# Kernel optimization log

Measured on AMD Instinct MI355X. Metric: run time of the kernel, lower is better.

The kernel has to match this reference:

```python
import jax, jax.numpy as jnp
import numpy as np

B, N, C, H = 2, 4096, 512, 8
D = C // H          # head dim = 64
EPS = 1e-5          # nn.LayerNorm default eps


def _layernorm(x, gamma, beta):
    m = jnp.mean(x, axis=-1, keepdims=True)
    v = jnp.var(x, axis=-1, keepdims=True)
    return (x - m) * jax.lax.rsqrt(v + EPS) * gamma + beta


def setup_inputs() -> dict:
    key = jax.random.key(0)
    k_x, k_w = jax.random.split(key, 2)
    return {
        "x": jax.random.normal(k_x, (B, N, C), dtype=jnp.float32),
        "w_qkv": jax.random.normal(k_w, (C, 3 * C), dtype=jnp.float32) * 0.02,
        "b_qkv": jnp.zeros((3 * C,), dtype=jnp.float32),
        "g_pre": jnp.ones((C,), dtype=jnp.float32),
        "beta_pre": jnp.zeros((C,), dtype=jnp.float32),
        "g_post": jnp.ones((C,), dtype=jnp.float32),
        "beta_post": jnp.zeros((C,), dtype=jnp.float32),
    }


def reference(x, w_qkv, b_qkv, g_pre, beta_pre, g_post, beta_post):
    b, n, c = x.shape
    xn = _layernorm(x, g_pre, beta_pre)                       # pre_norm (x is reassigned in source)
    qkv = (xn @ w_qkv + b_qkv).reshape(b, n, 3, H, D)
    qkv = jnp.transpose(qkv, (2, 0, 3, 1, 4))                 # [3, B, H, N, D]
    q, k, v = qkv[0], qkv[1], qkv[2]
    scale = D ** (-0.5)
    attn = jnp.einsum('bhnd,bhmd->bhnm', q, k) * scale        # [B, H, N, N]
    soft = jax.nn.softmax(attn, axis=-1)
    val = jnp.einsum('bhnm,bhmd->bhnd', soft, v)              # [B, H, N, D]
    val = jnp.transpose(val, (0, 2, 1, 3)).reshape(b, n, c)   # [B, N, C]
    val = _layernorm(val, g_post, beta_post)                  # post_norm
    return xn + val                                            # residual uses pre-normed x (faithful)
```

## Files before the change

### kernel.cpp

```cpp
#include <hip/hip_runtime.h>

#define BB   2
#define NN   4096
#define CC   512
#define HH   8
#define DD   64
#define MR   8192
#define NC3  1536
#define PS   4194304

typedef __attribute__((ext_vector_type(8))) short short8;
typedef __attribute__((ext_vector_type(4))) float floatx4;

__device__ inline unsigned short f2bf(float f) {
  unsigned int u = __float_as_uint(f);
  u = (u + 0x7fffu + ((u >> 16) & 1u)) >> 16;
  return (unsigned short)u;
}

__device__ inline unsigned int pack_bf2(float a, float b) {
  unsigned int ua = __float_as_uint(a) + 0x8000u;
  unsigned int ub = __float_as_uint(b) + 0x8000u;
  return (ub & 0xffff0000u) | (ua >> 16);
}

__device__ inline floatx4 fzero4() { floatx4 z = {0.f, 0.f, 0.f, 0.f}; return z; }

__device__ inline void async_cp16(const void* g, void* l) {
  __builtin_amdgcn_global_load_lds(
      (const __attribute__((address_space(1))) unsigned int*)g,
      (__attribute__((address_space(3))) unsigned int*)l, 16, 0, 0);
}

__global__ __launch_bounds__(256) void convert_w_kernel(
    const float* __restrict__ w, unsigned short* __restrict__ wt) {
  __shared__ short T[64][68];
  int bn = blockIdx.x;
  int bk = blockIdx.y;
  int tid = threadIdx.x;
  for (int p = 0; p < 4; p++) {
    int k = p * 16 + (tid >> 4);
    int n4 = (tid & 15) * 4;
    float4 v = *(const float4*)&w[(size_t)(bk * 64 + k) * NC3 + bn * 64 + n4];
    T[n4 + 0][k] = (short)f2bf(v.x);
    T[n4 + 1][k] = (short)f2bf(v.y);
    T[n4 + 2][k] = (short)f2bf(v.z);
    T[n4 + 3][k] = (short)f2bf(v.w);
  }
  __syncthreads();
  for (int p = 0; p < 2; p++) {
    int n = p * 32 + (tid >> 3);
    int k8 = (tid & 7) * 8;
    uint4 v = *(uint4*)&T[n][k8];
    *(uint4*)&wt[(size_t)(bn * 64 + n) * 512 + bk * 64 + k8] = v;
  }
}

__global__ __launch_bounds__(256) void pre_ln_kernel(
    const float* __restrict__ x, const float* __restrict__ g,
    const float* __restrict__ be, float* __restrict__ xn,
    unsigned short* __restrict__ xnb) {
  int wv = threadIdx.x >> 6, lane = threadIdx.x & 63;
  int row = blockIdx.x * 4 + wv;
  const float4* xr = (const float4*)(x + (size_t)row * CC);
  float4 v0 = xr[lane];
  float4 v1 = xr[64 + lane];
  float s  = (v0.x + v0.y) + (v0.z + v0.w) + (v1.x + v1.y) + (v1.z + v1.w);
  float sq = (v0.x * v0.x + v0.y * v0.y) + (v0.z * v0.z + v0.w * v0.w) +
             (v1.x * v1.x + v1.y * v1.y) + (v1.z * v1.z + v1.w * v1.w);
  for (int off = 1; off < 64; off <<= 1) {
    s  += __shfl_xor(s,  off, 64);
    sq += __shfl_xor(sq, off, 64);
  }
  float mean = s * (1.0f / CC);
  float var  = sq * (1.0f / CC) - mean * mean;
  float rstd = rsqrtf(var + 1e-5f);
  const float4* gg = (const float4*)g;
  const float4* bb = (const float4*)be;
  float4 g0 = gg[lane], g1 = gg[64 + lane];
  float4 b0 = bb[lane], b1 = bb[64 + lane];
  float4 o0, o1;
  o0.x = (v0.x - mean) * rstd * g0.x + b0.x;
  o0.y = (v0.y - mean) * rstd * g0.y + b0.y;
  o0.z = (v0.z - mean) * rstd * g0.z + b0.z;
  o0.w = (v0.w - mean) * rstd * g0.w + b0.w;
  o1.x = (v1.x - mean) * rstd * g1.x + b1.x;
  o1.y = (v1.y - mean) * rstd * g1.y + b1.y;
  o1.z = (v1.z - mean) * rstd * g1.z + b1.z;
  o1.w = (v1.w - mean) * rstd * g1.w + b1.w;
  size_t base = (size_t)row * CC;
  ((float4*)(xn + base))[lane] = o0;
  ((float4*)(xn + base))[64 + lane] = o1;
  uint2 u0, u1;
  u0.x = pack_bf2(o0.x, o0.y); u0.y = pack_bf2(o0.z, o0.w);
  u1.x = pack_bf2(o1.x, o1.y); u1.y = pack_bf2(o1.z, o1.w);
  *(uint2*)&xnb[base + 4 * lane] = u0;
  *(uint2*)&xnb[base + 256 + 4 * lane] = u1;
}

#define QSCALE 0.180336879f

__global__ __launch_bounds__(256) void qkv_gemm_kernel(
    const unsigned short* __restrict__ xnb, const unsigned short* __restrict__ wt,
    const float* __restrict__ bias, unsigned short* __restrict__ qkvb) {
  __shared__ __align__(16) char smem[65536];
  short (*Asb[2])[64];
  short (*Bsb[2])[64];
  Asb[0] = (short (*)[64])smem;
  Bsb[0] = (short (*)[64])(smem + 16384);
  Asb[1] = (short (*)[64])(smem + 32768);
  Bsb[1] = (short (*)[64])(smem + 49152);
  short (*T)[136] = (short (*)[136])smem;

  int tn = blockIdx.x;
  int tm = blockIdx.y;
  int tid = threadIdx.x;
  int wv = tid >> 6, lane = tid & 63;
  int quad = lane >> 4, l16 = lane & 15;
  int wm = wv >> 1, wn = wv & 1;
  int l7 = l16 & 7;

  int kr = lane >> 3;
  int kg = (lane & 7) ^ kr;

  floatx4 acc[4][4];
  for (int i = 0; i < 4; i++) for (int j = 0; j < 4; j++) acc[i][j] = fzero4();

  for (int i = 0; i < 4; i++) {
    int rb = i * 32 + wv * 8;
    async_cp16(&xnb[(size_t)(tm * 128 + rb + kr) * 512 + kg * 8], &Asb[0][rb][0]);
    async_cp16(&wt [(size_t)(tn * 128 + rb + kr) * 512 + kg * 8], &Bsb[0][rb][0]);
  }

  for (int it = 0; it < 8; it++) {
    __syncthreads();
    short (*As)[64] = Asb[it & 1];
    short (*Bs)[64] = Bsb[it & 1];
    if (it < 7) {
      int kn = (it + 1) * 64;
      short (*An)[64] = Asb[(it + 1) & 1];
      short (*Bn)[64] = Bsb[(it + 1) & 1];
      for (int i = 0; i < 4; i++) {
        int rb = i * 32 + wv * 8;
        async_cp16(&xnb[(size_t)(tm * 128 + rb + kr) * 512 + kn + kg * 8], &An[rb][0]);
        async_cp16(&wt [(size_t)(tn * 128 + rb + kr) * 512 + kn + kg * 8], &Bn[rb][0]);
      }
    }
    for (int kk = 0; kk < 2; kk++) {
      short8 a[4], b[4];
      for (int mt = 0; mt < 4; mt++)
        a[mt] = *(const short8*)&As[wm * 64 + mt * 16 + l16][((kk * 4 + quad) ^ l7) * 8];
      for (int nt = 0; nt < 4; nt++)
        b[nt] = *(const short8*)&Bs[wn * 64 + nt * 16 + l16][((kk * 4 + quad) ^ l7) * 8];
      for (int mt = 0; mt < 4; mt++)
        for (int nt = 0; nt < 4; nt++)
          acc[mt][nt] = __builtin_amdgcn_mfma_f32_16x16x32_bf16(a[mt], b[nt], acc[mt][nt], 0, 0, 0);
    }
  }
  __syncthreads();

  int part = tn >> 2;
  int b = tm >> 5;
  int tloc = (tm & 31) * 128;

  if (part < 2) {
    for (int nt = 0; nt < 4; nt++) {
      int coll = wn * 64 + nt * 16 + l16;
      float bv = bias[tn * 128 + coll];
      for (int mt = 0; mt < 4; mt++) {
        int rowb = wm * 64 + mt * 16 + quad * 4;
        for (int r = 0; r < 4; r++) {
          float v = acc[mt][nt][r] + bv;
          if (part == 0) v *= QSCALE;
          T[rowb + r][coll] = (short)f2bf(v);
        }
      }
    }
    __syncthreads();
    int h0 = (tn & 3) * 2;
    for (int it = 0; it < 8; it++) {
      int row = it * 16 + (tid >> 4);
      int l = tid & 15;
      uint4 vv = *(uint4*)&T[row][l * 8];
      int h = h0 + (l >> 3), d = (l & 7) * 8;
      size_t idx = (size_t)part * PS +
                   ((size_t)((b * 8 + h) * 4096 + tloc + row)) * 64 + d;
      *(uint4*)&qkvb[idx] = vv;
    }
  } else {
    for (int nt = 0; nt < 4; nt++) {
      int coll = wn * 64 + nt * 16 + l16;
      float bv = bias[tn * 128 + coll];
      for (int mt = 0; mt < 4; mt++) {
        int rowb = wm * 64 + mt * 16 + quad * 4;
        uint2 w;
        w.x = pack_bf2(acc[mt][nt][0] + bv, acc[mt][nt][1] + bv);
        w.y = pack_bf2(acc[mt][nt][2] + bv, acc[mt][nt][3] + bv);
        *(uint2*)&T[coll][rowb] = w;
      }
    }
    __syncthreads();
    for (int it = 0; it < 8; it++) {
      int vrow = it * 16 + (tid >> 4);
      int l = tid & 15;
      uint4 vv = *(uint4*)&T[vrow][l * 8];
      int gj = tn * 128 + vrow;
      int h = (gj >> 6) & 7, d = gj & 63;
      size_t idx = 2 * (size_t)PS +
                   ((size_t)((b * 8 + h) * 64 + d)) * 4096 + tloc + l * 8;
      *(uint4*)&qkvb[idx] = vv;
    }
  }
}

#define SMEM_ATT (16384 + 32768 + 18432)

__global__ __launch_bounds__(256, 2) void attn_kernel(
    const unsigned short* __restrict__ qkvb, float* __restrict__ val) {
  __shared__ __align__(16) char smem[SMEM_ATT];
  short (*Ks)[64]   = (short (*)[64])smem;
  short (*Vt0)[128] = (short (*)[128])(smem + 16384);
  short (*Vt1)[128] = (short (*)[128])(smem + 32768);
  short (*Psl)[72]  = (short (*)[72])(smem + 49152);
  float (*slab)[68] = (float (*)[68])smem;

  int bh = blockIdx.y;
  int qb = blockIdx.x * 128;
  int tid = threadIdx.x;
  int wv = tid >> 6, lane = tid & 63, quad = lane >> 4, l16 = lane & 15;
  int l7 = l16 & 7;
  const unsigned short* Qg = qkvb + (size_t)bh * NN * DD;
  const unsigned short* Kg = qkvb + (size_t)PS + (size_t)bh * NN * DD;
  const unsigned short* Vg = qkvb + 2 * (size_t)PS + (size_t)bh * DD * NN;

  int kr = lane >> 3;
  int kg = (lane & 7) ^ kr;
  int vr = lane >> 4;
  int vgr = (lane & 15) ^ ((wv * 4 + vr) & 15);

  for (int i = 0; i < 4; i++) {
    int rowbase = i * 32 + wv * 8;
    async_cp16(&Qg[(size_t)(qb + rowbase + kr) * 64 + kg * 8], &Ks[rowbase][0]);
  }
  __syncthreads();
  short8 qf[2][2];
  for (int g = 0; g < 2; g++)
    for (int kk = 0; kk < 2; kk++)
      qf[g][kk] = *(const short8*)&Ks[wv * 32 + g * 16 + l16][((kk * 4 + quad) ^ l7) * 8];
  __syncthreads();

  for (int i = 0; i < 4; i++) {
    int rb = i * 32 + wv * 8;
    async_cp16(&Kg[(size_t)(rb + kr) * 64 + kg * 8], &Ks[rb][0]);
  }
  for (int i = 0; i < 4; i++) {
    int rb = i * 16 + wv * 4;
    async_cp16(&Vg[(size_t)(rb + vr) * NN + vgr * 8], &Vt0[rb][0]);
  }

  floatx4 o[2][4];
  for (int g = 0; g < 2; g++) for (int dt = 0; dt < 4; dt++) o[g][dt] = fzero4();
  float ls[2] = {0.0f, 0.0f};

  short* psrow0 = &Psl[wv * 32 + l16][0];
  short* psrow1 = &Psl[wv * 32 + 16 + l16][0];

  for (int kt = 0; kt < 32; kt++) {
    __syncthreads();
    short (*Vc)[128] = (kt & 1) ? Vt1 : Vt0;
    short (*Vn)[128] = (kt & 1) ? Vt0 : Vt1;
    if (kt < 31) {
      int kn = (kt + 1) * 128;
      for (int i = 0; i < 4; i++) {
        int rb = i * 16 + wv * 4;
        async_cp16(&Vg[(size_t)(rb + vr) * NN + kn + vgr * 8], &Vn[rb][0]);
      }
    }

    floatx4 s[2][8];
    for (int nt = 0; nt < 8; nt++) {
      short8 kf0 = *(const short8*)&Ks[nt * 16 + l16][((quad) ^ l7) * 8];
      short8 kf1 = *(const short8*)&Ks[nt * 16 + l16][((4 + quad) ^ l7) * 8];
      floatx4 s0 = fzero4(), s1 = fzero4();
      s0 = __builtin_amdgcn_mfma_f32_16x16x32_bf16(kf0, qf[0][0], s0, 0, 0, 0);
      s0 = __builtin_amdgcn_mfma_f32_16x16x32_bf16(kf1, qf[0][1], s0, 0, 0, 0);
      s1 = __builtin_amdgcn_mfma_f32_16x16x32_bf16(kf0, qf[1][0], s1, 0, 0, 0);
      s1 = __builtin_amdgcn_mfma_f32_16x16x32_bf16(kf1, qf[1][1], s1, 0, 0, 0);
      s[0][nt] = s0;
      s[1][nt] = s1;
    }
    __syncthreads();
    if (kt < 31) {
      int kn = (kt + 1) * 128;
      for (int i = 0; i < 4; i++) {
        int rb = i * 32 + wv * 8;
        async_cp16(&Kg[(size_t)(kn + rb + kr) * 64 + kg * 8], &Ks[rb][0]);
      }
    }

    for (int hf = 0; hf < 2; hf++) {
      for (int n4 = 0; n4 < 4; n4++) {
        int nt = hf * 4 + n4;
        float p00 = __builtin_amdgcn_exp2f(s[0][nt][0]);
        float p01 = __builtin_amdgcn_exp2f(s[0][nt][1]);
        float p02 = __builtin_amdgcn_exp2f(s[0][nt][2]);
        float p03 = __builtin_amdgcn_exp2f(s[0][nt][3]);
        float p10 = __builtin_amdgcn_exp2f(s[1][nt][0]);
        float p11 = __builtin_amdgcn_exp2f(s[1][nt][1]);
        float p12 = __builtin_amdgcn_exp2f(s[1][nt][2]);
        float p13 = __builtin_amdgcn_exp2f(s[1][nt][3]);
        ls[0] += (p00 + p01) + (p02 + p03);
        ls[1] += (p10 + p11) + (p12 + p13);
        uint2 w0, w1;
        w0.x = pack_bf2(p00, p01);  w0.y = pack_bf2(p02, p03);
        w1.x = pack_bf2(p10, p11);  w1.y = pack_bf2(p12, p13);
        *(uint2*)&psrow0[n4 * 16 + quad * 4] = w0;
        *(uint2*)&psrow1[n4 * 16 + quad * 4] = w1;
      }
      for (int ks = 0; ks < 2; ks++) {
        int ksg = hf * 2 + ks;
        short8 pa0 = *(const short8*)&Psl[wv * 32 + l16][ks * 32 + quad * 8];
        short8 pa1 = *(const short8*)&Psl[wv * 32 + 16 + l16][ks * 32 + quad * 8];
        for (int dt = 0; dt < 4; dt++) {
          short8 vb = *(const short8*)&Vc[dt * 16 + l16][((ksg * 4 + quad) ^ l16) * 8];
          o[0][dt] = __builtin_amdgcn_mfma_f32_16x16x32_bf16(vb, pa0, o[0][dt], 0, 0, 0);
          o[1][dt] = __builtin_amdgcn_mfma_f32_16x16x32_bf16(vb, pa1, o[1][dt], 0, 0, 0);
        }
      }
    }
  }

  for (int g = 0; g < 2; g++) {
    ls[g] += __shfl_xor(ls[g], 16, 64);
    ls[g] += __shfl_xor(ls[g], 32, 64);
  }

  __syncthreads();
  for (int g = 0; g < 2; g++) {
    float inv = 1.0f / ls[g];
    int q = wv * 32 + g * 16 + l16;
    for (int dt = 0; dt < 4; dt++)
      for (int r = 0; r < 4; r++)
        slab[q][dt * 16 + quad * 4 + r] = o[g][dt][r] * inv;
  }
  __syncthreads();
  int b = bh >> 3, h = bh & 7;
  for (int it = 0; it < 8; it++) {
    int row = it * 16 + (tid >> 4);
    int col4 = (tid & 15) * 4;
    float4 vv = *(float4*)&slab[row][col4];
    *(float4*)&val[((size_t)(b * 4096 + qb + row)) * 512 + h * 64 + col4] = vv;
  }
}

__global__ __launch_bounds__(256) void post_ln_kernel(
    const float* __restrict__ valp, const float* __restrict__ xn,
    const float* __restrict__ g, const float* __restrict__ be,
    float* __restrict__ out) {
  int wv = threadIdx.x >> 6, lane = threadIdx.x & 63;
  int row = blockIdx.x * 4 + wv;
  const float4* vr = (const float4*)(valp + (size_t)row * CC);
  float4 v0 = vr[lane];
  float4 v1 = vr[64 + lane];
  float s  = (v0.x + v0.y) + (v0.z + v0.w) + (v1.x + v1.y) + (v1.z + v1.w);
  float sq = (v0.x * v0.x + v0.y * v0.y) + (v0.z * v0.z + v0.w * v0.w) +
             (v1.x * v1.x + v1.y * v1.y) + (v1.z * v1.z + v1.w * v1.w);
  for (int off = 1; off < 64; off <<= 1) {
    s  += __shfl_xor(s,  off, 64);
    sq += __shfl_xor(sq, off, 64);
  }
  float mean = s * (1.0f / CC);
  float var  = sq * (1.0f / CC) - mean * mean;
  float rstd = rsqrtf(var + 1e-5f);
  const float4* gg = (const float4*)g;
  const float4* bb = (const float4*)be;
  float4 g0 = gg[lane], g1 = gg[64 + lane];
  float4 b0 = bb[lane], b1 = bb[64 + lane];
  const float4* xr = (const float4*)(xn + (size_t)row * CC);
  float4 x0 = xr[lane], x1 = xr[64 + lane];
  float4 o0, o1;
  o0.x = (v0.x - mean) * rstd * g0.x + b0.x + x0.x;
  o0.y = (v0.y - mean) * rstd * g0.y + b0.y + x0.y;
  o0.z = (v0.z - mean) * rstd * g0.z + b0.z + x0.z;
  o0.w = (v0.w - mean) * rstd * g0.w + b0.w + x0.w;
  o1.x = (v1.x - mean) * rstd * g1.x + b1.x + x1.x;
  o1.y = (v1.y - mean) * rstd * g1.y + b1.y + x1.y;
  o1.z = (v1.z - mean) * rstd * g1.z + b1.z + x1.z;
  o1.w = (v1.w - mean) * rstd * g1.w + b1.w + x1.w;
  ((float4*)(out + (size_t)row * CC))[lane] = o0;
  ((float4*)(out + (size_t)row * CC))[64 + lane] = o1;
}

extern "C" void kernel_launch(void* const* d_in, const int* in_sizes, int n_in,
                              void* d_out, int out_size, void* d_ws, size_t ws_size,
                              hipStream_t stream) {
  const float* x       = (const float*)d_in[0];
  const float* w_qkv   = (const float*)d_in[1];
  const float* b_qkv   = (const float*)d_in[2];
  const float* g_pre   = (const float*)d_in[3];
  const float* be_pre  = (const float*)d_in[4];
  const float* g_post  = (const float*)d_in[5];
  const float* be_post = (const float*)d_in[6];
  float* out = (float*)d_out;

  float* xn  = (float*)d_ws;
  float* val = xn + 4194304;
  unsigned short* xnb  = (unsigned short*)(val + 4194304);
  unsigned short* qkvb = xnb + 4194304;
  unsigned short* wt   = qkvb + 3 * (size_t)PS;

  convert_w_kernel<<<dim3(24, 8), 256, 0, stream>>>(w_qkv, wt);
  pre_ln_kernel<<<2048, 256, 0, stream>>>(x, g_pre, be_pre, xn, xnb);
  qkv_gemm_kernel<<<dim3(12, 64), 256, 0, stream>>>(xnb, wt, b_qkv, qkvb);
  attn_kernel<<<dim3(32, 16), 256, 0, stream>>>(qkvb, val);
  post_ln_kernel<<<2048, 256, 0, stream>>>(val, xn, g_post, be_post, out);
}
```

Before: 206.3 us.

## Split attention keys across two blocks, keep P in registers, drop fp32 xn

Attention now splits the key range in two (grid z=2). Each half writes unnormalized partial outputs and row sums, and post-LN merges them and normalizes. The P tile no longer goes through LDS: it is packed into registers and fed to 16x16x16 bf16 MFMAs using the score accumulator layout directly. This frees shared memory so occupancy can rise to 3 blocks per SM. The fp32 xn buffer is gone and the residual is read back from bf16 xnb, which trades a loss of residual precision for less memory traffic. Extra partial-output traffic (two fp32 val buffers) is added.

```diff
diff --git a/kernel.cpp b/kernel.cpp
--- a/kernel.cpp
+++ b/kernel.cpp
@@ -10,7 +10,20 @@
 #define PS   4194304
 
 typedef __attribute__((ext_vector_type(8))) short short8;
+typedef __attribute__((ext_vector_type(4))) short short4v;
 typedef __attribute__((ext_vector_type(4))) float floatx4;
+
+#if __has_builtin(__builtin_amdgcn_mfma_f32_16x16x16_bf16_1k)
+#define MFMA16(a, b, c) __builtin_amdgcn_mfma_f32_16x16x16_bf16_1k(a, b, c, 0, 0, 0)
+#elif __has_builtin(__builtin_amdgcn_mfma_f32_16x16x16_bf16)
+#define MFMA16(a, b, c) __builtin_amdgcn_mfma_f32_16x16x16_bf16(a, b, c, 0, 0, 0)
+#else
+__device__ inline floatx4 mfma16_asm(short4v a, short4v b, floatx4 c) {
+  asm volatile("v_mfma_f32_16x16x16_bf16 %0, %1, %2, %0" : "+v"(c) : "v"(a), "v"(b));
+  return c;
+}
+#define MFMA16(a, b, c) mfma16_asm(a, b, c)
+#endif
 
 __device__ inline unsigned short f2bf(float f) {
   unsigned int u = __float_as_uint(f);
@@ -22,6 +35,13 @@
   unsigned int ua = __float_as_uint(a) + 0x8000u;
   unsigned int ub = __float_as_uint(b) + 0x8000u;
   return (ub & 0xffff0000u) | (ua >> 16);
+}
+
+__device__ inline short4v pack_bf4(float a, float b, float c, float d) {
+  union { unsigned int u[2]; short4v v; } t;
+  t.u[0] = pack_bf2(a, b);
+  t.u[1] = pack_bf2(c, d);
+  return t.v;
 }
 
 __device__ inline floatx4 fzero4() { floatx4 z = {0.f, 0.f, 0.f, 0.f}; return z; }
@@ -58,8 +78,7 @@
 
 __global__ __launch_bounds__(256) void pre_ln_kernel(
     const float* __restrict__ x, const float* __restrict__ g,
-    const float* __restrict__ be, float* __restrict__ xn,
-    unsigned short* __restrict__ xnb) {
+    const float* __restrict__ be, unsigned short* __restrict__ xnb) {
   int wv = threadIdx.x >> 6, lane = threadIdx.x & 63;
   int row = blockIdx.x * 4 + wv;
   const float4* xr = (const float4*)(x + (size_t)row * CC);
@@ -89,8 +108,6 @@
   o1.z = (v1.z - mean) * rstd * g1.z + b1.z;
   o1.w = (v1.w - mean) * rstd * g1.w + b1.w;
   size_t base = (size_t)row * CC;
-  ((float4*)(xn + base))[lane] = o0;
-  ((float4*)(xn + base))[64 + lane] = o1;
   uint2 u0, u1;
   u0.x = pack_bf2(o0.x, o0.y); u0.y = pack_bf2(o0.z, o0.w);
   u1.x = pack_bf2(o1.x, o1.y); u1.y = pack_bf2(o1.z, o1.w);
@@ -213,25 +230,28 @@
   }
 }
 
-#define SMEM_ATT (16384 + 32768 + 18432)
-
-__global__ __launch_bounds__(256, 2) void attn_kernel(
-    const unsigned short* __restrict__ qkvb, float* __restrict__ val) {
+#define SMEM_ATT (16384 + 32768)
+
+__global__ __launch_bounds__(256, 3) void attn_kernel(
+    const unsigned short* __restrict__ qkvb, float* __restrict__ valp,
+    float* __restrict__ lsum) {
   __shared__ __align__(16) char smem[SMEM_ATT];
   short (*Ks)[64]   = (short (*)[64])smem;
   short (*Vt0)[128] = (short (*)[128])(smem + 16384);
   short (*Vt1)[128] = (short (*)[128])(smem + 32768);
-  short (*Psl)[72]  = (short (*)[72])(smem + 49152);
   float (*slab)[68] = (float (*)[68])smem;
 
   int bh = blockIdx.y;
   int qb = blockIdx.x * 128;
+  int ksp = blockIdx.z;
   int tid = threadIdx.x;
   int wv = tid >> 6, lane = tid & 63, quad = lane >> 4, l16 = lane & 15;
   int l7 = l16 & 7;
   const unsigned short* Qg = qkvb + (size_t)bh * NN * DD;
-  const unsigned short* Kg = qkvb + (size_t)PS + (size_t)bh * NN * DD;
-  const unsigned short* Vg = qkvb + 2 * (size_t)PS + (size_t)bh * DD * NN;
+  const unsigned short* Kg = qkvb + (size_t)PS + (size_t)bh * NN * DD +
+                             (size_t)ksp * 2048 * DD;
+  const unsigned short* Vg = qkvb + 2 * (size_t)PS + (size_t)bh * DD * NN +
+                             (size_t)ksp * 2048;
 
   int kr = lane >> 3;
   int kg = (lane & 7) ^ kr;
@@ -239,8 +259,8 @@
   int vgr = (lane & 15) ^ ((wv * 4 + vr) & 15);
 
   for (int i = 0; i < 4; i++) {
-    int rowbase = i * 32 + wv * 8;
-    async_cp16(&Qg[(size_t)(qb + rowbase + kr) * 64 + kg * 8], &Ks[rowbase][0]);
+    int rb = i * 32 + wv * 8;
+    async_cp16(&Qg[(size_t)(qb + rb + kr) * 64 + kg * 8], &Ks[rb][0]);
   }
   __syncthreads();
   short8 qf[2][2];
@@ -262,14 +282,11 @@
   for (int g = 0; g < 2; g++) for (int dt = 0; dt < 4; dt++) o[g][dt] = fzero4();
   float ls[2] = {0.0f, 0.0f};
 
-  short* psrow0 = &Psl[wv * 32 + l16][0];
-  short* psrow1 = &Psl[wv * 32 + 16 + l16][0];
-
-  for (int kt = 0; kt < 32; kt++) {
+  for (int kt = 0; kt < 16; kt++) {
     __syncthreads();
     short (*Vc)[128] = (kt & 1) ? Vt1 : Vt0;
     short (*Vn)[128] = (kt & 1) ? Vt0 : Vt1;
-    if (kt < 31) {
+    if (kt < 15) {
       int kn = (kt + 1) * 128;
       for (int i = 0; i < 4; i++) {
         int rb = i * 16 + wv * 4;
@@ -290,7 +307,7 @@
       s[1][nt] = s1;
     }
     __syncthreads();
-    if (kt < 31) {
+    if (kt < 15) {
       int kn = (kt + 1) * 128;
       for (int i = 0; i < 4; i++) {
         int rb = i * 32 + wv * 8;
@@ -298,34 +315,24 @@
       }
     }
 
-    for (int hf = 0; hf < 2; hf++) {
-      for (int n4 = 0; n4 < 4; n4++) {
-        int nt = hf * 4 + n4;
-        float p00 = __builtin_amdgcn_exp2f(s[0][nt][0]);
-        float p01 = __builtin_amdgcn_exp2f(s[0][nt][1]);
-        float p02 = __builtin_amdgcn_exp2f(s[0][nt][2]);
-        float p03 = __builtin_amdgcn_exp2f(s[0][nt][3]);
-        float p10 = __builtin_amdgcn_exp2f(s[1][nt][0]);
-        float p11 = __builtin_amdgcn_exp2f(s[1][nt][1]);
-        float p12 = __builtin_amdgcn_exp2f(s[1][nt][2]);
-        float p13 = __builtin_amdgcn_exp2f(s[1][nt][3]);
-        ls[0] += (p00 + p01) + (p02 + p03);
-        ls[1] += (p10 + p11) + (p12 + p13);
-        uint2 w0, w1;
-        w0.x = pack_bf2(p00, p01);  w0.y = pack_bf2(p02, p03);
-        w1.x = pack_bf2(p10, p11);  w1.y = pack_bf2(p12, p13);
-        *(uint2*)&psrow0[n4 * 16 + quad * 4] = w0;
-        *(uint2*)&psrow1[n4 * 16 + quad * 4] = w1;
-      }
-      for (int ks = 0; ks < 2; ks++) {
-        int ksg = hf * 2 + ks;
-        short8 pa0 = *(const short8*)&Psl[wv * 32 + l16][ks * 32 + quad * 8];
-        short8 pa1 = *(const short8*)&Psl[wv * 32 + 16 + l16][ks * 32 + quad * 8];
-        for (int dt = 0; dt < 4; dt++) {
-          short8 vb = *(const short8*)&Vc[dt * 16 + l16][((ksg * 4 + quad) ^ l16) * 8];
-          o[0][dt] = __builtin_amdgcn_mfma_f32_16x16x32_bf16(vb, pa0, o[0][dt], 0, 0, 0);
-          o[1][dt] = __builtin_amdgcn_mfma_f32_16x16x32_bf16(vb, pa1, o[1][dt], 0, 0, 0);
-        }
+    for (int nt = 0; nt < 8; nt++) {
+      float p00 = __builtin_amdgcn_exp2f(s[0][nt][0]);
+      float p01 = __builtin_amdgcn_exp2f(s[0][nt][1]);
+      float p02 = __builtin_amdgcn_exp2f(s[0][nt][2]);
+      float p03 = __builtin_amdgcn_exp2f(s[0][nt][3]);
+      float p10 = __builtin_amdgcn_exp2f(s[1][nt][0]);
+      float p11 = __builtin_amdgcn_exp2f(s[1][nt][1]);
+      float p12 = __builtin_amdgcn_exp2f(s[1][nt][2]);
+      float p13 = __builtin_amdgcn_exp2f(s[1][nt][3]);
+      ls[0] += (p00 + p01) + (p02 + p03);
+      ls[1] += (p10 + p11) + (p12 + p13);
+      short4v pa0 = pack_bf4(p00, p01, p02, p03);
+      short4v pa1 = pack_bf4(p10, p11, p12, p13);
+      for (int dt = 0; dt < 4; dt++) {
+        short4v vb = *(const short4v*)&Vc[dt * 16 + l16]
+            [(((nt * 2 + (quad >> 1)) ^ l16) * 8) + (quad & 1) * 4];
+        o[0][dt] = MFMA16(vb, pa0, o[0][dt]);
+        o[1][dt] = MFMA16(vb, pa1, o[1][dt]);
       }
     }
   }
@@ -334,34 +341,53 @@
     ls[g] += __shfl_xor(ls[g], 16, 64);
     ls[g] += __shfl_xor(ls[g], 32, 64);
   }
+  float* lrow = lsum + (size_t)(ksp * 16 + bh) * 4096 + qb;
+  if (lane < 16) {
+    lrow[wv * 32 + l16] = ls[0];
+    lrow[wv * 32 + 16 + l16] = ls[1];
+  }
 
   __syncthreads();
   for (int g = 0; g < 2; g++) {
-    float inv = 1.0f / ls[g];
     int q = wv * 32 + g * 16 + l16;
     for (int dt = 0; dt < 4; dt++)
       for (int r = 0; r < 4; r++)
-        slab[q][dt * 16 + quad * 4 + r] = o[g][dt][r] * inv;
+        slab[q][dt * 16 + quad * 4 + r] = o[g][dt][r];
   }
   __syncthreads();
   int b = bh >> 3, h = bh & 7;
+  float* myval = valp + (size_t)ksp * MR * CC;
   for (int it = 0; it < 8; it++) {
     int row = it * 16 + (tid >> 4);
     int col4 = (tid & 15) * 4;
     float4 vv = *(float4*)&slab[row][col4];
-    *(float4*)&val[((size_t)(b * 4096 + qb + row)) * 512 + h * 64 + col4] = vv;
+    *(float4*)&myval[((size_t)(b * 4096 + qb + row)) * 512 + h * 64 + col4] = vv;
   }
 }
 
 __global__ __launch_bounds__(256) void post_ln_kernel(
-    const float* __restrict__ valp, const float* __restrict__ xn,
+    const float* __restrict__ valp, const float* __restrict__ lsum,
+    const unsigned short* __restrict__ xnb,
     const float* __restrict__ g, const float* __restrict__ be,
     float* __restrict__ out) {
   int wv = threadIdx.x >> 6, lane = threadIdx.x & 63;
   int row = blockIdx.x * 4 + wv;
-  const float4* vr = (const float4*)(valp + (size_t)row * CC);
-  float4 v0 = vr[lane];
-  float4 v1 = vr[64 + lane];
+  int b = row >> 12, q = row & 4095;
+  const float4* p1 = (const float4*)(valp + (size_t)row * CC);
+  const float4* p2 = (const float4*)(valp + (size_t)MR * CC + (size_t)row * CC);
+  float4 a0 = p1[lane], a1 = p1[64 + lane];
+  float4 c0 = p2[lane], c1 = p2[64 + lane];
+  int h0 = lane >> 4, h1 = 4 + (lane >> 4);
+  float lt0 = lsum[(size_t)(b * 8 + h0) * 4096 + q] +
+              lsum[(size_t)(16 + b * 8 + h0) * 4096 + q];
+  float lt1 = lsum[(size_t)(b * 8 + h1) * 4096 + q] +
+              lsum[(size_t)(16 + b * 8 + h1) * 4096 + q];
+  float i0 = 1.0f / lt0, i1 = 1.0f / lt1;
+  float4 v0, v1;
+  v0.x = (a0.x + c0.x) * i0;  v0.y = (a0.y + c0.y) * i0;
+  v0.z = (a0.z + c0.z) * i0;  v0.w = (a0.w + c0.w) * i0;
+  v1.x = (a1.x + c1.x) * i1;  v1.y = (a1.y + c1.y) * i1;
+  v1.z = (a1.z + c1.z) * i1;  v1.w = (a1.w + c1.w) * i1;
   float s  = (v0.x + v0.y) + (v0.z + v0.w) + (v1.x + v1.y) + (v1.z + v1.w);
   float sq = (v0.x * v0.x + v0.y * v0.y) + (v0.z * v0.z + v0.w * v0.w) +
              (v1.x * v1.x + v1.y * v1.y) + (v1.z * v1.z + v1.w * v1.w);
@@ -376,19 +402,25 @@
   const float4* bb = (const float4*)be;
   float4 g0 = gg[lane], g1 = gg[64 + lane];
   float4 b0 = bb[lane], b1 = bb[64 + lane];
-  const float4* xr = (const float4*)(xn + (size_t)row * CC);
-  float4 x0 = xr[lane], x1 = xr[64 + lane];
+  size_t base = (size_t)row * CC;
+  uint2 x0 = *(const uint2*)&xnb[base + 4 * lane];
+  uint2 x1 = *(const uint2*)&xnb[base + 256 + 4 * lane];
+  float4 r0, r1;
+  r0.x = __uint_as_float(x0.x << 16);  r0.y = __uint_as_float(x0.x & 0xffff0000u);
+  r0.z = __uint_as_float(x0.y << 16);  r0.w = __uint_as_float(x0.y & 0xffff0000u);
+  r1.x = __uint_as_float(x1.x << 16);  r1.y = __uint_as_float(x1.x & 0xffff0000u);
+  r1.z = __uint_as_float(x1.y << 16);  r1.w = __uint_as_float(x1.y & 0xffff0000u);
   float4 o0, o1;
-  o0.x = (v0.x - mean) * rstd * g0.x + b0.x + x0.x;
-  o0.y = (v0.y - mean) * rstd * g0.y + b0.y + x0.y;
-  o0.z = (v0.z - mean) * rstd * g0.z + b0.z + x0.z;
-  o0.w = (v0.w - mean) * rstd * g0.w + b0.w + x0.w;
-  o1.x = (v1.x - mean) * rstd * g1.x + b1.x + x1.x;
-  o1.y = (v1.y - mean) * rstd * g1.y + b1.y + x1.y;
-  o1.z = (v1.z - mean) * rstd * g1.z + b1.z + x1.z;
-  o1.w = (v1.w - mean) * rstd * g1.w + b1.w + x1.w;
-  ((float4*)(out + (size_t)row * CC))[lane] = o0;
-  ((float4*)(out + (size_t)row * CC))[64 + lane] = o1;
+  o0.x = (v0.x - mean) * rstd * g0.x + b0.x + r0.x;
+  o0.y = (v0.y - mean) * rstd * g0.y + b0.y + r0.y;
+  o0.z = (v0.z - mean) * rstd * g0.z + b0.z + r0.z;
+  o0.w = (v0.w - mean) * rstd * g0.w + b0.w + r0.w;
+  o1.x = (v1.x - mean) * rstd * g1.x + b1.x + r1.x;
+  o1.y = (v1.y - mean) * rstd * g1.y + b1.y + r1.y;
+  o1.z = (v1.z - mean) * rstd * g1.z + b1.z + r1.z;
+  o1.w = (v1.w - mean) * rstd * g1.w + b1.w + r1.w;
+  ((float4*)(out + base))[lane] = o0;
+  ((float4*)(out + base))[64 + lane] = o1;
 }
 
 extern "C" void kernel_launch(void* const* d_in, const int* in_sizes, int n_in,
@@ -403,15 +435,15 @@
   const float* be_post = (const float*)d_in[6];
   float* out = (float*)d_out;
 
-  float* xn  = (float*)d_ws;
-  float* val = xn + 4194304;
-  unsigned short* xnb  = (unsigned short*)(val + 4194304);
+  float* val  = (float*)d_ws;
+  float* lsum = val + 2 * (size_t)MR * CC;
+  unsigned short* xnb  = (unsigned short*)(lsum + 2 * 16 * 4096);
   unsigned short* qkvb = xnb + 4194304;
   unsigned short* wt   = qkvb + 3 * (size_t)PS;
 
   convert_w_kernel<<<dim3(24, 8), 256, 0, stream>>>(w_qkv, wt);
-  pre_ln_kernel<<<2048, 256, 0, stream>>>(x, g_pre, be_pre, xn, xnb);
+  pre_ln_kernel<<<2048, 256, 0, stream>>>(x, g_pre, be_pre, xnb);
   qkv_gemm_kernel<<<dim3(12, 64), 256, 0, stream>>>(xnb, wt, b_qkv, qkvb);
-  attn_kernel<<<dim3(32, 16), 256, 0, stream>>>(qkvb, val);
-  post_ln_kernel<<<2048, 256, 0, stream>>>(val, xn, g_post, be_post, out);
-}
+  attn_kernel<<<dim3(32, 16, 2), 256, 0, stream>>>(qkvb, val, lsum);
+  post_ln_kernel<<<2048, 256, 0, stream>>>(val, lsum, xnb, g_post, be_post, out);
+}
```

After: 203.8 us. Within noise of the previous version (-1.2%).
